# Performance work log

Hardware: AMD Instinct MI355X
Metric: run time of the kernel (lower is better)

## Reference

```python
import jax, jax.numpy as jnp
import numpy as np

NUM_HEADS = 16
HEAD_SIZE = 64
MAX_POS = 2048  # config.max_position_embeddings


def setup_inputs() -> dict:
    key = jax.random.key(0)
    ks = jax.random.split(key, 8)
    B, Lq, Lk, D = 4, 1024, 2048, 1024
    s = 1.0 / np.sqrt(D)
    return {
        "hidden_states": jax.random.normal(ks[0], (B, Lk, D), jnp.float32),
        "query_hidden_states": jax.random.normal(ks[1], (B, Lq, D), jnp.float32),
        "attention_mask": jnp.zeros((B, 1, 1, Lk), jnp.float32),
        "Wq": jax.random.normal(ks[2], (D, D), jnp.float32) * s,
        "bq": jnp.zeros((D,), jnp.float32),
        "Wk": jax.random.normal(ks[3], (D, D), jnp.float32) * s,
        "bk": jnp.zeros((D,), jnp.float32),
        "Wv": jax.random.normal(ks[4], (D, D), jnp.float32) * s,
        "bv": jnp.zeros((D,), jnp.float32),
        "dist_emb": jax.random.normal(ks[5], (2 * MAX_POS - 1, HEAD_SIZE), jnp.float32) * 0.02,
    }


def _split_heads(x):
    # [B, L, H*Dh] -> [B, H, L, Dh]
    B, L, _ = x.shape
    return x.reshape(B, L, NUM_HEADS, HEAD_SIZE).transpose(0, 2, 1, 3)


def reference(hidden_states, query_hidden_states, attention_mask, Wq, bq, Wk, bk, Wv, bv, dist_emb):
    # Linear projections (torch Linear: x @ W.T + b)
    q = _split_heads(query_hidden_states @ Wq.T + bq)   # [B,H,Lq,Dh]
    k = _split_heads(hidden_states @ Wk.T + bk)          # [B,H,Lk,Dh]
    v = _split_heads(hidden_states @ Wv.T + bv)          # [B,H,Lk,Dh]

    scores = jnp.einsum('bhld,bhrd->bhlr', q, k)         # [B,H,Lq,Lk]

    # relative_key_query positional scores
    Lq, Lk = q.shape[2], k.shape[2]
    distance = jnp.arange(Lq)[:, None] - jnp.arange(Lk)[None, :]
    pe = dist_emb[distance + MAX_POS - 1]                # [Lq,Lk,Dh]
    scores = scores + jnp.einsum('bhld,lrd->bhlr', q, pe) + jnp.einsum('bhrd,lrd->bhlr', k, pe)

    scores = scores / np.sqrt(HEAD_SIZE) + attention_mask
    probs = jax.nn.softmax(scores, axis=-1)              # dropout p=0 (eval)
    ctx = jnp.einsum('bhlr,bhrd->bhld', probs, v)        # [B,H,Lq,Dh]
    B = ctx.shape[0]
    return ctx.transpose(0, 2, 1, 3).reshape(B, Lq, NUM_HEADS * HEAD_SIZE)
```

## Files before the change

### kernel.cpp

```cpp
#include <hip/hip_runtime.h>
#include <hip/hip_bf16.h>

#define B_   4
#define H_   16
#define LQ   1024
#define LK   2048
#define D_   1024
#define DH   64

typedef __attribute__((ext_vector_type(8))) short  short8;
typedef __attribute__((ext_vector_type(4))) float  float4_;
typedef __attribute__((ext_vector_type(4))) unsigned int uint4_;

static __device__ __forceinline__ float bf2f(unsigned short u) {
    unsigned int x = ((unsigned int)u) << 16;
    return __builtin_bit_cast(float, x);
}
static __device__ __forceinline__ unsigned short f2bf(float f) {
    unsigned int x = __builtin_bit_cast(unsigned int, f);
    unsigned int lsb = (x >> 16) & 1u;
    x += 0x7fffu + lsb;
    return (unsigned short)(x >> 16);
}
static __device__ __forceinline__ unsigned int pack2(float a, float b) {
    __hip_bfloat162 h = __float22bfloat162_rn(make_float2(a, b));
    unsigned int r;
    __builtin_memcpy(&r, &h, 4);
    return r;
}
template<int CTRL>
static __device__ __forceinline__ float dppmv(float x) {
    int i = __builtin_bit_cast(int, x);
    int r = __builtin_amdgcn_update_dpp(i, i, CTRL, 0xf, 0xf, false);
    return __builtin_bit_cast(float, r);
}

#define MFMA(a, b, c) __builtin_amdgcn_mfma_f32_16x16x32_bf16((a), (b), (c), 0, 0, 0)

#define GLOAD_LDS16(g, l) __builtin_amdgcn_global_load_lds( \
    (const __attribute__((address_space(1))) unsigned int*)(const void*)(g), \
    (__attribute__((address_space(3))) unsigned int*)(void*)(l), 16, 0, 0)

__global__ __launch_bounds__(256) void conv_kernel(
    const float* __restrict__ Wq, const float* __restrict__ Wk,
    const float* __restrict__ Wv, const float* __restrict__ Eg,
    const float* __restrict__ Xq, const float* __restrict__ Xk,
    unsigned short* __restrict__ cWq, unsigned short* __restrict__ cWk,
    unsigned short* __restrict__ cWv, unsigned short* __restrict__ cEb,
    unsigned short* __restrict__ cXq, unsigned short* __restrict__ cXk)
{
    int bid = blockIdx.x;
    const float* src; unsigned short* dst; int nch;
    if (bid < 512)       { src = Wq; dst = cWq;              nch = 131072;  }
    else if (bid < 1024) { src = Wk; dst = cWk; bid -= 512;  nch = 131072;  }
    else if (bid < 1536) { src = Wv; dst = cWv; bid -= 1024; nch = 131072;  }
    else if (bid < 1664) { src = Eg; dst = cEb; bid -= 1536; nch = 32760;   }
    else if (bid < 3712) { src = Xq; dst = cXq; bid -= 1664; nch = 524288;  }
    else                 { src = Xk; dst = cXk; bid -= 3712; nch = 1048576; }
    int ch = bid * 256 + threadIdx.x;
    if (ch >= nch) return;
    const float* s = src + (size_t)ch * 8;
    float4_ v0 = *(const float4_*)s, v1 = *(const float4_*)(s + 4);
    uint4_ o;
    o[0] = pack2(v0[0], v0[1]); o[1] = pack2(v0[2], v0[3]);
    o[2] = pack2(v1[0], v1[1]); o[3] = pack2(v1[2], v1[3]);
    *(uint4_*)(dst + (size_t)ch * 8) = o;
}

__global__ __launch_bounds__(256) void proj_kernel(
    const unsigned short* __restrict__ Xq, const unsigned short* __restrict__ Xk,
    const unsigned short* __restrict__ Wq, const float* __restrict__ bq,
    const unsigned short* __restrict__ Wk, const float* __restrict__ bk,
    const unsigned short* __restrict__ Wv, const float* __restrict__ bv,
    unsigned short* __restrict__ Qh, unsigned short* __restrict__ Kh,
    unsigned short* __restrict__ VT)
{
    __shared__ short smem[32768];
    short* A0 = smem;
    short* B0 = smem + 8192;
    short* A1 = smem + 16384;
    short* B1 = smem + 24576;
    short* Cs = smem;

    int bid = blockIdx.x;
    int which, tm, tn;
    const unsigned short *X; const float* bias; const unsigned short* W;
    if (bid < 256)      { which = 0; int t = bid;       tm = t >> 3; tn = t & 7; X = Xq; W = Wq; bias = bq; }
    else if (bid < 768) { which = 1; int t = bid - 256; tm = t >> 3; tn = t & 7; X = Xk; W = Wk; bias = bk; }
    else                { which = 2; int t = bid - 768; tm = t >> 3; tn = t & 7; X = Xk; W = Wv; bias = bv; }

    int tid  = threadIdx.x;
    int wave = tid >> 6, lane = tid & 63;
    int wr = (wave >> 1) * 64, wc = (wave & 1) * 64;
    int m0 = tm * 128, n0 = tn * 128;

    float4_ acc[4][4];
    for (int a = 0; a < 4; ++a) for (int c = 0; c < 4; ++c) acc[a][c] = (float4_)0.0f;

    int rl = lane >> 3;
    int chs = (lane & 7) ^ rl;
    const unsigned short* Asrc = X + (size_t)(m0 + wave * 32 + rl) * D_ + (chs << 3);
    const unsigned short* Bsrc = W + (size_t)(n0 + wave * 32 + rl) * D_ + (chs << 3);

    int lrow = lane & 15, lk8 = (lane >> 4) * 8;
    int swz = lane & 7;

    auto stage = [&](short* Ad, short* Bd, int kt) {
        int k0 = kt * 64;
        #pragma unroll
        for (int c = 0; c < 4; ++c) {
            GLOAD_LDS16(Asrc + (size_t)(c * 8) * D_ + k0, &Ad[(wave * 32 + c * 8) * 64]);
            GLOAD_LDS16(Bsrc + (size_t)(c * 8) * D_ + k0, &Bd[(wave * 32 + c * 8) * 64]);
        }
    };
    auto compute = [&](const short* Aa, const short* Bb) {
        #pragma unroll
        for (int kk = 0; kk < 64; kk += 32) {
            int cgrp = (kk + lk8) >> 3;
            int coff = ((cgrp ^ swz) << 3);
            short8 af[4], bfr[4];
            #pragma unroll
            for (int rt = 0; rt < 4; ++rt)
                af[rt]  = *(const short8*)(&Aa[(wr + rt * 16 + lrow) * 64 + coff]);
            #pragma unroll
            for (int ct = 0; ct < 4; ++ct)
                bfr[ct] = *(const short8*)(&Bb[(wc + ct * 16 + lrow) * 64 + coff]);
            #pragma unroll
            for (int rt = 0; rt < 4; ++rt)
                #pragma unroll
                for (int ct = 0; ct < 4; ++ct)
                    acc[rt][ct] = MFMA(af[rt], bfr[ct], acc[rt][ct]);
        }
    };

    stage(A0, B0, 0);
    __syncthreads();
    for (int kt = 0; kt < 16; kt += 2) {
        if (kt + 1 < 16) stage(A1, B1, kt + 1);
        compute(A0, B0);
        __syncthreads();
        if (kt + 2 < 16) stage(A0, B0, kt + 2);
        compute(A1, B1);
        __syncthreads();
    }

    int lrow4 = (lane >> 4) * 4, lcol = lane & 15;
    if (which < 2) {
        int lsh = (which == 0) ? 10 : 11;
        int Lm1 = (1 << lsh) - 1;
        unsigned short* dst = (which == 0) ? Qh : Kh;
        for (int rt = 0; rt < 4; ++rt)
            for (int ct = 0; ct < 4; ++ct)
                for (int i = 0; i < 4; ++i) {
                    int m = m0 + wr + rt * 16 + lrow4 + i;
                    int n = n0 + wc + ct * 16 + lcol;
                    float v = acc[rt][ct][i] + bias[n];
                    int b = m >> lsh, s = m & Lm1;
                    int h = n >> 6, d = n & 63;
                    dst[((size_t)((b * H_ + h) << lsh) + (size_t)s) * DH + d] = f2bf(v);
                }
    } else {
        for (int rt = 0; rt < 4; ++rt)
            for (int ct = 0; ct < 4; ++ct)
                for (int i = 0; i < 4; ++i) {
                    int rl2 = wr + rt * 16 + lrow4 + i;
                    int cl  = wc + ct * 16 + lcol;
                    float v = acc[rt][ct][i] + bias[n0 + cl];
                    Cs[cl * 136 + rl2] = (short)f2bf(v);
                }
        __syncthreads();
        int b = m0 >> 11, r0 = m0 & 2047;
        int c = tid >> 1, half = tid & 1;
        int n = n0 + c, h = n >> 6, d = n & 63;
        unsigned short* dstp = VT + ((size_t)(b * H_ + h) * DH + d) * LK + r0 + half * 64;
        for (int j = 0; j < 8; ++j) {
            uint4_ v = *(const uint4_*)(&Cs[c * 136 + half * 64 + j * 8]);
            *(uint4_*)(dstp + j * 8) = v;
        }
    }
}

__global__ __launch_bounds__(256, 2) void attn_kernel(
    const unsigned short* __restrict__ Qh, const unsigned short* __restrict__ Kh,
    const unsigned short* __restrict__ VT, const unsigned short* __restrict__ Eb,
    const float* __restrict__ mask, float* __restrict__ out)
{
    __shared__ short smem[22144];
    short* Qs  = smem;
    short* Ks  = smem;
    short* VTs = smem + 4608;
    short* Ps  = smem + 9216;
    unsigned int* Gqk = (unsigned int*)(smem + 13824);
    short* Gs  = smem + 13824;

    int bid = blockIdx.x;
    int l0 = (bid & 15) * 64;
    int bh = bid >> 4;
    int b  = bh >> 4, h = bh & 15;
    int tid = threadIdx.x, wave = tid >> 6, lane = tid & 63;
    int lr = lane & 15, lk8 = (lane >> 4) * 8, lr4 = (lane >> 4) * 4;

    for (int i = 0; i < 2; ++i) {
        int idx = tid + 256 * i, row = idx >> 3, g = (idx & 7) * 8;
        *(uint4_*)(&Qs[row * 72 + g]) =
            *(const uint4_*)(Qh + ((size_t)(bh * LQ + l0 + row)) * DH + g);
    }
    __syncthreads();
    short8 aq0 = *(const short8*)(&Qs[(wave * 16 + lr) * 72 + lk8]);
    short8 aq1 = *(const short8*)(&Qs[(wave * 16 + lr) * 72 + 32 + lk8]);

    float m_i[4], l_i[4];
    float4_ Oacc[4];
    for (int i = 0; i < 4; ++i) { m_i[i] = -1e30f; l_i[i] = 0.f; Oacc[i] = (float4_)0.f; }

    const unsigned short* Kbase = Kh + (size_t)bh * LK * DH;
    const unsigned short* Vbase = VT + (size_t)bh * DH * LK;

    int srow = tid >> 3;
    int sg   = (tid & 7) * 8;

    uint4_ kr0, kr1, vr0, vr1;
    auto load_kv = [&](int nit) {
        int r0_ = nit * 64;
        kr0 = *(const uint4_*)(Kbase + (size_t)(r0_ + srow) * DH + sg);
        kr1 = *(const uint4_*)(Kbase + (size_t)(r0_ + srow + 32) * DH + sg);
        vr0 = *(const uint4_*)(Vbase + (size_t)srow * LK + r0_ + sg);
        vr1 = *(const uint4_*)(Vbase + (size_t)(srow + 32) * LK + r0_ + sg);
    };
    load_kv(0);

    short8 ef[8][2];
    {
        const unsigned short* ep = Eb + (size_t)(l0 + 1984 + lr) * DH + lk8;
        #pragma unroll
        for (int t = 0; t < 8; ++t) {
            ef[t][0] = *(const short8*)(ep + (size_t)t * 16 * DH);
            ef[t][1] = *(const short8*)(ep + (size_t)t * 16 * DH + 32);
        }
    }

    for (int it2 = 0; it2 < 32; it2 += 2) {
      #pragma unroll
      for (int sub = 0; sub < 2; ++sub) {
        const int it = it2 + sub;
        const int p4 = sub * 4;
        int r0 = it * 64;

        __syncthreads();
        *(uint4_*)(&Ks[srow * 72 + sg])         = kr0;
        *(uint4_*)(&Ks[(srow + 32) * 72 + sg])  = kr1;
        *(uint4_*)(&VTs[srow * 72 + sg])        = vr0;
        *(uint4_*)(&VTs[(srow + 32) * 72 + sg]) = vr1;
        __syncthreads();
        if (it < 31) load_kv(it + 1);

        short8 ak0, ak1;
        float4_ Sacc[4];
        #pragma unroll
        for (int c = 0; c < 4; ++c) {
            short8 b0 = *(const short8*)(&Ks[(c * 16 + lr) * 72 + lk8]);
            short8 b1 = *(const short8*)(&Ks[(c * 16 + lr) * 72 + 32 + lk8]);
            float4_ s = (float4_)0.f;
            s = MFMA(aq0, b0, s);
            s = MFMA(aq1, b1, s);
            Sacc[c] = s;
            if (c == 0 || c == wave) { ak0 = b0; ak1 = b1; }
        }

        #pragma unroll
        for (int t = 0; t < 8; ++t) {
            int dq = t - wave, dk = t - 3 + wave;
            bool needq = (unsigned)dq < 5u, needk = (unsigned)dk < 5u;
            if (!(needq || needk)) continue;
            short8 e0 = ef[t ^ p4][0], e1 = ef[t ^ p4][1];
            int u = t * 16 + lr;
            if (needq) {
                float4_ g = (float4_)0.f;
                g = MFMA(aq0, e0, g); g = MFMA(aq1, e1, g);
                unsigned int p0 = pack2(g[0], g[1]), p1 = pack2(g[2], g[3]);
                #pragma unroll
                for (int i = 0; i < 4; ++i) {
                    int row = wave * 16 + lr4 + i;
                    unsigned int w32 = (i >> 1) ? p1 : p0;
                    unsigned short vq = (unsigned short)((i & 1) ? (w32 >> 16) : (w32 & 0xffff));
                    int tr = row - u + 63;
                    if ((unsigned)tr < 64u)
                        Gs[(row * 65 + tr) * 2] = (short)vq;
                }
            }
            if (needk) {
                float4_ gg = (float4_)0.f;
                gg = MFMA(ak0, e0, gg); gg = MFMA(ak1, e1, gg);
                unsigned int q0 = pack2(gg[0], gg[1]), q1 = pack2(gg[2], gg[3]);
                #pragma unroll
                for (int i = 0; i < 4; ++i) {
                    int row = wave * 16 + lr4 + i;
                    unsigned int w32 = (i >> 1) ? q1 : q0;
                    unsigned short vk = (unsigned short)((i & 1) ? (w32 >> 16) : (w32 & 0xffff));
                    int tl = u + row - 63;
                    if ((unsigned)tl < 64u)
                        Gs[(tl * 65 + row) * 2 + 1] = (short)vk;
                }
            }
        }
        __syncthreads();

        if (it < 31) {
            const unsigned short* ep =
                Eb + (size_t)(l0 + 1984 - 64 * (it + 1) + lr) * DH + lk8;
            #pragma unroll
            for (int t = 0; t < 4; ++t) {
                ef[t ^ p4 ^ 4][0] = *(const short8*)(ep + (size_t)t * 16 * DH);
                ef[t ^ p4 ^ 4][1] = *(const short8*)(ep + (size_t)t * 16 * DH + 32);
            }
        }

        float mk[4];
        for (int c = 0; c < 4; ++c) mk[c] = mask[b * LK + r0 + c * 16 + lr];
        #pragma unroll
        for (int i = 0; i < 4; ++i) {
            int tl = wave * 16 + lr4 + i;
            const unsigned int* gr = Gqk + tl * 65 + lr;
            unsigned int gva[4];
            gva[0] = gr[0]; gva[1] = gr[16]; gva[2] = gr[32]; gva[3] = gr[48];
            float scv[4], mx = -1e30f;
            #pragma unroll
            for (int c = 0; c < 4; ++c) {
                float sq = bf2f((unsigned short)(gva[c] & 0xffff));
                float sk = bf2f((unsigned short)(gva[c] >> 16));
                float sc = (Sacc[c][i] + sq + sk) * 0.125f + mk[c];
                scv[c] = sc;
                mx = fmaxf(mx, sc);
            }
            mx = fmaxf(mx, dppmv<0xB1>(mx));
            mx = fmaxf(mx, dppmv<0x4E>(mx));
            mx = fmaxf(mx, dppmv<0x141>(mx));
            mx = fmaxf(mx, dppmv<0x140>(mx));
            float mnew = fmaxf(m_i[i], mx);
            float alpha = __expf(m_i[i] - mnew);
            m_i[i] = mnew;
            float e0 = __expf(scv[0] - mnew), e1 = __expf(scv[1] - mnew);
            float e2 = __expf(scv[2] - mnew), e3 = __expf(scv[3] - mnew);
            unsigned int p01 = pack2(e0, e1), p23 = pack2(e2, e3);
            float rs = bf2f((unsigned short)(p01 & 0xffff)) + bf2f((unsigned short)(p01 >> 16))
                     + bf2f((unsigned short)(p23 & 0xffff)) + bf2f((unsigned short)(p23 >> 16));
            rs += dppmv<0xB1>(rs);
            rs += dppmv<0x4E>(rs);
            rs += dppmv<0x141>(rs);
            rs += dppmv<0x140>(rs);
            l_i[i] = l_i[i] * alpha + rs;
            for (int nt = 0; nt < 4; ++nt) Oacc[nt][i] *= alpha;
            short* Pr = Ps + tl * 72;
            Pr[ 0 + lr] = (short)(unsigned short)(p01 & 0xffff);
            Pr[16 + lr] = (short)(unsigned short)(p01 >> 16);
            Pr[32 + lr] = (short)(unsigned short)(p23 & 0xffff);
            Pr[48 + lr] = (short)(unsigned short)(p23 >> 16);
        }
        const short* Pa = Ps + (wave * 16 + lr) * 72;
        short8 ap0 = *(const short8*)(Pa + lk8);
        short8 ap1 = *(const short8*)(Pa + 32 + lk8);
        #pragma unroll
        for (int nt = 0; nt < 4; ++nt) {
            short8 v0 = *(const short8*)(&VTs[(nt * 16 + lr) * 72 + lk8]);
            short8 v1 = *(const short8*)(&VTs[(nt * 16 + lr) * 72 + 32 + lk8]);
            Oacc[nt] = MFMA(ap0, v0, Oacc[nt]);
            Oacc[nt] = MFMA(ap1, v1, Oacc[nt]);
        }
      }
    }

    for (int nt = 0; nt < 4; ++nt)
        for (int i = 0; i < 4; ++i) {
            int row = l0 + wave * 16 + lr4 + i;
            int col = h * 64 + nt * 16 + lr;
            out[(size_t)(b * LQ + row) * D_ + col] = Oacc[nt][i] / l_i[i];
        }
}

extern "C" void kernel_launch(void* const* d_in, const int* in_sizes, int n_in,
                              void* d_out, int out_size, void* d_ws, size_t ws_size,
                              hipStream_t stream) {
    (void)in_sizes; (void)n_in; (void)out_size; (void)ws_size;
    const float* Xk   = (const float*)d_in[0];
    const float* Xq   = (const float*)d_in[1];
    const float* mask = (const float*)d_in[2];
    const float* Wq   = (const float*)d_in[3];
    const float* bq   = (const float*)d_in[4];
    const float* Wk   = (const float*)d_in[5];
    const float* bk   = (const float*)d_in[6];
    const float* Wv   = (const float*)d_in[7];
    const float* bv   = (const float*)d_in[8];
    const float* Eg   = (const float*)d_in[9];

    unsigned short* Qh  = (unsigned short*)d_ws;
    unsigned short* Kh  = Qh  + (size_t)4194304;
    unsigned short* VT  = Kh  + (size_t)8388608;
    unsigned short* cWq = VT  + (size_t)8388608;
    unsigned short* cWk = cWq + (size_t)1048576;
    unsigned short* cWv = cWk + (size_t)1048576;
    unsigned short* cEb = cWv + (size_t)1048576;
    unsigned short* cXq = cEb + (size_t)262144;
    unsigned short* cXk = (unsigned short*)d_out;
    float* o = (float*)d_out;

    conv_kernel<<<7808, 256, 0, stream>>>(Wq, Wk, Wv, Eg, Xq, Xk,
                                          cWq, cWk, cWv, cEb, cXq, cXk);
    proj_kernel<<<1280, 256, 0, stream>>>(cXq, cXk, cWq, bq, cWk, bk, cWv, bv, Qh, Kh, VT);
    attn_kernel<<<1024, 256, 0, stream>>>(Qh, Kh, VT, cEb, mask, o);
}
```

Before: 443.3 us.

## Double-buffer K/V tiles via direct global-to-LDS loads with XOR swizzle

Replaces the register-staged K/V loading (global to registers, then registers to LDS between two barriers) with direct global-to-LDS loads into a double-buffered LDS region. The next tile is prefetched into the alternate buffer while the current one is consumed. An XOR swizzle on unpadded 64-element rows replaces the 72-element padding to avoid bank conflicts. This removes one barrier per iteration and the register round-trip, but raises LDS usage, which could limit occupancy, and relies on GLOAD_LDS16 completion semantics being handled correctly at the barrier.

```diff
diff --git a/kernel.cpp b/kernel.cpp
--- a/kernel.cpp
+++ b/kernel.cpp
@@ -185,13 +185,10 @@
     const unsigned short* __restrict__ VT, const unsigned short* __restrict__ Eb,
     const float* __restrict__ mask, float* __restrict__ out)
 {
-    __shared__ short smem[22144];
-    short* Qs  = smem;
-    short* Ks  = smem;
-    short* VTs = smem + 4608;
-    short* Ps  = smem + 9216;
-    unsigned int* Gqk = (unsigned int*)(smem + 13824);
-    short* Gs  = smem + 13824;
+    __shared__ short smem[29312];
+    short* Gs = smem + 16384;
+    unsigned int* Gqk = (unsigned int*)(smem + 16384);
+    short* Ps = smem + 24704;
 
     int bid = blockIdx.x;
     int l0 = (bid & 15) * 64;
@@ -199,36 +196,41 @@
     int b  = bh >> 4, h = bh & 15;
     int tid = threadIdx.x, wave = tid >> 6, lane = tid & 63;
     int lr = lane & 15, lk8 = (lane >> 4) * 8, lr4 = (lane >> 4) * 4;
-
-    for (int i = 0; i < 2; ++i) {
-        int idx = tid + 256 * i, row = idx >> 3, g = (idx & 7) * 8;
-        *(uint4_*)(&Qs[row * 72 + g]) =
-            *(const uint4_*)(Qh + ((size_t)(bh * LQ + l0 + row)) * DH + g);
+    int rl8 = lane >> 3;
+    int sch = ((lane & 7) ^ rl8) << 3;
+    int co0 = ((lane >> 4) ^ (lr & 7)) << 3;
+
+    const unsigned short* Kbase = Kh + (size_t)bh * LK * DH;
+    const unsigned short* Vbase = VT + (size_t)bh * DH * LK;
+
+    #pragma unroll
+    for (int c = 0; c < 2; ++c) {
+        int rw = c * 32 + wave * 8;
+        GLOAD_LDS16(Qh + ((size_t)(bh * LQ + l0 + rw + rl8)) * DH + sch,
+                    &smem[rw * 64]);
     }
     __syncthreads();
-    short8 aq0 = *(const short8*)(&Qs[(wave * 16 + lr) * 72 + lk8]);
-    short8 aq1 = *(const short8*)(&Qs[(wave * 16 + lr) * 72 + 32 + lk8]);
+    short8 aq0 = *(const short8*)(&smem[(wave * 16 + lr) * 64 + co0]);
+    short8 aq1 = *(const short8*)(&smem[(wave * 16 + lr) * 64 + (co0 ^ 32)]);
+    __syncthreads();
+
+    auto stage_kv = [&](int nit, int buf) {
+        int r0_ = nit * 64;
+        short* Kb = smem + buf * 8192;
+        short* Vb = smem + 4096 + buf * 8192;
+        #pragma unroll
+        for (int c = 0; c < 2; ++c) {
+            int rw = c * 32 + wave * 8;
+            GLOAD_LDS16(Kbase + (size_t)(r0_ + rw + rl8) * DH + sch, &Kb[rw * 64]);
+            GLOAD_LDS16(Vbase + (size_t)(rw + rl8) * LK + r0_ + sch, &Vb[rw * 64]);
+        }
+    };
+    stage_kv(0, 0);
 
     float m_i[4], l_i[4];
     float4_ Oacc[4];
     for (int i = 0; i < 4; ++i) { m_i[i] = -1e30f; l_i[i] = 0.f; Oacc[i] = (float4_)0.f; }
 
-    const unsigned short* Kbase = Kh + (size_t)bh * LK * DH;
-    const unsigned short* Vbase = VT + (size_t)bh * DH * LK;
-
-    int srow = tid >> 3;
-    int sg   = (tid & 7) * 8;
-
-    uint4_ kr0, kr1, vr0, vr1;
-    auto load_kv = [&](int nit) {
-        int r0_ = nit * 64;
-        kr0 = *(const uint4_*)(Kbase + (size_t)(r0_ + srow) * DH + sg);
-        kr1 = *(const uint4_*)(Kbase + (size_t)(r0_ + srow + 32) * DH + sg);
-        vr0 = *(const uint4_*)(Vbase + (size_t)srow * LK + r0_ + sg);
-        vr1 = *(const uint4_*)(Vbase + (size_t)(srow + 32) * LK + r0_ + sg);
-    };
-    load_kv(0);
-
     short8 ef[8][2];
     {
         const unsigned short* ep = Eb + (size_t)(l0 + 1984 + lr) * DH + lk8;
@@ -238,6 +240,7 @@
             ef[t][1] = *(const short8*)(ep + (size_t)t * 16 * DH + 32);
         }
     }
+    __syncthreads();
 
     for (int it2 = 0; it2 < 32; it2 += 2) {
       #pragma unroll
@@ -245,21 +248,18 @@
         const int it = it2 + sub;
         const int p4 = sub * 4;
         int r0 = it * 64;
-
-        __syncthreads();
-        *(uint4_*)(&Ks[srow * 72 + sg])         = kr0;
-        *(uint4_*)(&Ks[(srow + 32) * 72 + sg])  = kr1;
-        *(uint4_*)(&VTs[srow * 72 + sg])        = vr0;
-        *(uint4_*)(&VTs[(srow + 32) * 72 + sg]) = vr1;
-        __syncthreads();
-        if (it < 31) load_kv(it + 1);
+        const int cur = sub;
+        const short* Kb = smem + cur * 8192;
+        const short* Vb = smem + 4096 + cur * 8192;
+
+        if (it < 31) stage_kv(it + 1, cur ^ 1);
 
         short8 ak0, ak1;
         float4_ Sacc[4];
         #pragma unroll
         for (int c = 0; c < 4; ++c) {
-            short8 b0 = *(const short8*)(&Ks[(c * 16 + lr) * 72 + lk8]);
-            short8 b1 = *(const short8*)(&Ks[(c * 16 + lr) * 72 + 32 + lk8]);
+            short8 b0 = *(const short8*)(&Kb[(c * 16 + lr) * 64 + co0]);
+            short8 b1 = *(const short8*)(&Kb[(c * 16 + lr) * 64 + (co0 ^ 32)]);
             float4_ s = (float4_)0.f;
             s = MFMA(aq0, b0, s);
             s = MFMA(aq1, b1, s);
@@ -361,11 +361,12 @@
         short8 ap1 = *(const short8*)(Pa + 32 + lk8);
         #pragma unroll
         for (int nt = 0; nt < 4; ++nt) {
-            short8 v0 = *(const short8*)(&VTs[(nt * 16 + lr) * 72 + lk8]);
-            short8 v1 = *(const short8*)(&VTs[(nt * 16 + lr) * 72 + 32 + lk8]);
+            short8 v0 = *(const short8*)(&Vb[(nt * 16 + lr) * 64 + co0]);
+            short8 v1 = *(const short8*)(&Vb[(nt * 16 + lr) * 64 + (co0 ^ 32)]);
             Oacc[nt] = MFMA(ap0, v0, Oacc[nt]);
             Oacc[nt] = MFMA(ap1, v1, Oacc[nt]);
         }
+        __syncthreads();
       }
     }
 
```

New measurement: 438.7 us. No clear change (-1.0%).
